# Kernel optimization log

Hardware: AMD Instinct MI355X
Metric: run time of the kernel (lower is better)

Reference implementation:

```python
import jax, jax.numpy as jnp
import numpy as np

NUM_HEADS = 16
HEAD_DIM = 128
EMBED_DIM = 2048
BASE = 10000.0


def rope(x, offset=0):
    # x: [b, h, n, d]  rotary positional embedding (lrpe_type=1)
    d = x.shape[-1]
    n = x.shape[-2]
    inv_freq = 1.0 / (BASE ** (jnp.arange(0, d, 2, dtype=jnp.float32) / d))  # [d/2]
    pos = jnp.arange(n, dtype=jnp.float32) + offset                          # [n]
    ang = pos[:, None] * inv_freq[None, :]                                   # [n, d/2]
    cos, sin = jnp.cos(ang), jnp.sin(ang)
    x1, x2 = x[..., 0::2], x[..., 1::2]
    out1 = x1 * cos - x2 * sin
    out2 = x1 * sin + x2 * cos
    return jnp.stack([out1, out2], axis=-1).reshape(x.shape)


def setup_inputs() -> dict:
    key = jax.random.key(0)
    ks = jax.random.split(key, 5)
    b, n = 2, 2048
    std = 0.02
    x = jax.random.normal(ks[0], (b, n, EMBED_DIM), dtype=jnp.float32)
    Wq = jax.random.normal(ks[1], (NUM_HEADS * HEAD_DIM, EMBED_DIM), dtype=jnp.float32) * std
    Wkv = jax.random.normal(ks[2], (2 * HEAD_DIM, EMBED_DIM), dtype=jnp.float32) * std
    Wkvh = jax.random.normal(ks[3], (2 * NUM_HEADS, EMBED_DIM), dtype=jnp.float32) * std
    Wo = jax.random.normal(ks[4], (EMBED_DIM, NUM_HEADS * HEAD_DIM), dtype=jnp.float32) * std
    return {"x": x, "Wq": Wq, "Wkv": Wkv, "Wkvh": Wkvh, "Wo": Wo}


def reference(x, Wq, Wkv, Wkvh, Wo):
    b, n, _ = x.shape
    h, d = NUM_HEADS, HEAD_DIM
    q = x @ Wq.T                     # [b, n, h*d]
    kv = x @ Wkv.T                   # [b, n, 2d]
    kvh = x @ Wkvh.T                 # [b, n, 2h]  (mpa_activation='none')
    k, v = kv[..., :d], kv[..., d:]
    k_head, v_head = kvh[..., :h], kvh[..., h:]
    # gate_type=0: per-token outer product broadcast of the single kv to all heads
    k = jnp.einsum('bnd,bnh->bhnd', k, k_head)
    v = jnp.einsum('bnd,bnh->bhnd', v, v_head)
    q = q.reshape(b, n, h, d).transpose(0, 2, 1, 3)  # [b, h, n, d]
    q = rope(q)
    k = rope(k)
    scale = 1.0 / jnp.sqrt(jnp.float32(d))
    scores = jnp.einsum('bhqd,bhkd->bhqk', q, k) * scale
    causal = jnp.tril(jnp.ones((n, n), dtype=bool))
    scores = jnp.where(causal, scores, -jnp.inf)
    attn = jax.nn.softmax(scores, axis=-1)
    o = jnp.einsum('bhqk,bhkd->bhqd', attn, v)
    o = o.transpose(0, 2, 1, 3).reshape(b, n, h * d)
    return o @ Wo.T
```

## Files before the change

kernel.cpp:

```cpp
#include <hip/hip_runtime.h>
#include <stdint.h>

#define BB 2
#define HH 16
#define NN 2048
#define DD 128
#define EE 2048
#define NQKV 2304

typedef short s16x8 __attribute__((ext_vector_type(8)));
typedef float fx4 __attribute__((ext_vector_type(4)));

static __device__ __forceinline__ unsigned short f2bf(float f) {
  unsigned u = __builtin_bit_cast(unsigned, f);
  u += 0x7fffu + ((u >> 16) & 1u);
  return (unsigned short)(u >> 16);
}
static __device__ __forceinline__ float bf2f(unsigned short h) {
  unsigned u = ((unsigned)h) << 16;
  return __builtin_bit_cast(float, u);
}
static __device__ __forceinline__ void gload_lds16(const void* g, void* l) {
  __builtin_amdgcn_global_load_lds(
      (const __attribute__((address_space(1))) unsigned int*)g,
      (__attribute__((address_space(3))) unsigned int*)l, 16, 0, 0);
}
static __device__ __forceinline__ unsigned cvt_pk_bf16(float lo, float hi) {
  unsigned w;
  asm("v_cvt_pk_bf16_f32 %0, %1, %2" : "=v"(w) : "v"(lo), "v"(hi));
  return w;
}

__global__ __launch_bounds__(256) void f2b_kernel(const float* __restrict__ in,
                                                  unsigned short* __restrict__ out,
                                                  int n4) {
  int i = blockIdx.x * 256 + threadIdx.x;
  if (i < n4) {
    float4 v = ((const float4*)in)[i];
    uint2 o;
    o.x = ((unsigned)f2bf(v.y) << 16) | f2bf(v.x);
    o.y = ((unsigned)f2bf(v.w) << 16) | f2bf(v.z);
    ((uint2*)out)[i] = o;
  }
}

#define GBM 128
#define GBN 128
#define GBK 32

__global__ __launch_bounds__(256) void gemm_bt(const unsigned short* __restrict__ A,
                                               const unsigned short* __restrict__ B,
                                               unsigned short* __restrict__ Cb,
                                               float* __restrict__ Cf,
                                               int M, int N, int K) {
  __shared__ alignas(16) unsigned short Alds[GBM * GBK];
  __shared__ alignas(16) unsigned short Blds[GBN * GBK];
  const int tid = threadIdx.x;
  const int wave = tid >> 6, lane = tid & 63;
  const int g = lane >> 4, lr = lane & 15;
  const int mtiles = M / GBM;
  const int mt = blockIdx.x % mtiles, nt = blockIdx.x / mtiles;
  const int m0 = mt * GBM, n0 = nt * GBN;
  const int wr = wave >> 1, wc = wave & 1;

  fx4 acc[4][4];
#pragma unroll
  for (int i = 0; i < 4; ++i)
#pragma unroll
    for (int j = 0; j < 4; ++j) acc[i][j] = (fx4){0.f, 0.f, 0.f, 0.f};

  const int srow = wave * 32 + (lane >> 2);
  const int scolb = (lane & 3) * 16;
  const unsigned char* Ag = (const unsigned char*)(A + (size_t)(m0 + srow) * K) + scolb;
  const unsigned char* Bg = (const unsigned char*)(B + (size_t)(n0 + srow) * K) + scolb;
  unsigned short* Al = Alds + wave * 32 * GBK;
  unsigned short* Bl = Blds + wave * 32 * GBK;
  const size_t rowb = (size_t)K * 2;

  for (int k0 = 0; k0 < K; k0 += GBK) {
    const unsigned char* ag = Ag + (size_t)k0 * 2;
    const unsigned char* bg = Bg + (size_t)k0 * 2;
    gload_lds16(ag, Al);
    gload_lds16(ag + 16 * rowb, Al + 16 * GBK);
    gload_lds16(bg, Bl);
    gload_lds16(bg + 16 * rowb, Bl + 16 * GBK);
    __syncthreads();
    s16x8 af[4], bf[4];
#pragma unroll
    for (int i = 0; i < 4; ++i)
      af[i] = *(const s16x8*)(Alds + (wr * 64 + i * 16 + lr) * GBK + 8 * g);
#pragma unroll
    for (int i = 0; i < 4; ++i)
      bf[i] = *(const s16x8*)(Blds + (wc * 64 + i * 16 + lr) * GBK + 8 * g);
#pragma unroll
    for (int i = 0; i < 4; ++i)
#pragma unroll
      for (int j = 0; j < 4; ++j)
        acc[i][j] = __builtin_amdgcn_mfma_f32_16x16x32_bf16(af[i], bf[j], acc[i][j], 0, 0, 0);
    __syncthreads();
  }
#pragma unroll
  for (int i = 0; i < 4; ++i) {
    int row = m0 + wr * 64 + i * 16 + 4 * g;
#pragma unroll
    for (int j = 0; j < 4; ++j) {
      int col = n0 + wc * 64 + j * 16 + lr;
#pragma unroll
      for (int r = 0; r < 4; ++r) {
        float v = acc[i][j][r];
        if (Cf) Cf[(size_t)(row + r) * N + col] = v;
        else    Cb[(size_t)(row + r) * N + col] = f2bf(v);
      }
    }
  }
}

__global__ __launch_bounds__(256) void kvh_mfma(const unsigned short* __restrict__ X,
                                                const unsigned short* __restrict__ Wb,
                                                float* __restrict__ out) {
  const int tid = threadIdx.x;
  const int wave = tid >> 6, lane = tid & 63;
  const int g = lane >> 4, lr = lane & 15;
  const int rowbase = blockIdx.x * 32 + (wave & 1) * 16;
  const int colbase = (wave >> 1) * 16;

  const unsigned short* xr = X + (size_t)(rowbase + lr) * EE + 8 * g;
  const unsigned short* wr = Wb + (size_t)(colbase + lr) * EE + 8 * g;

  fx4 acc = (fx4){0.f, 0.f, 0.f, 0.f};
#pragma unroll 8
  for (int k0 = 0; k0 < EE; k0 += 32) {
    s16x8 a = *(const s16x8*)(xr + k0);
    s16x8 b = *(const s16x8*)(wr + k0);
    acc = __builtin_amdgcn_mfma_f32_16x16x32_bf16(a, b, acc, 0, 0, 0);
  }
  const int j = colbase + lr;
  const int head = j & 15, sel = j >> 4;
#pragma unroll
  for (int r = 0; r < 4; ++r) {
    int m = rowbase + 4 * g + r;
    int b = m >> 11, n = m & (NN - 1);
    out[(((size_t)(b * HH + head)) * NN + n) * 2 + sel] = acc[r];
  }
}

__global__ __launch_bounds__(256) void rope_q(const unsigned short* __restrict__ qp,
                                              unsigned short* __restrict__ qo) {
  int idx = blockIdx.x * 256 + threadIdx.x;
  int i = idx & 63;
  int n = (idx >> 6) & (NN - 1);
  int bh = idx >> 17;
  int b = bh >> 4, h = bh & 15;
  unsigned v = *(const unsigned*)(qp + ((size_t)(b * NN + n) * NQKV + h * DD + 2 * i));
  float x1 = bf2f((unsigned short)(v & 0xffff));
  float x2 = bf2f((unsigned short)(v >> 16));
  float inv = __expf(-0.14391156831212787f * (float)i);
  float ang = (float)n * inv;
  float sn, cs;
  __sincosf(ang, &sn, &cs);
  float o1 = x1 * cs - x2 * sn, o2 = x1 * sn + x2 * cs;
  unsigned ov = ((unsigned)f2bf(o2) << 16) | f2bf(o1);
  *(unsigned*)(qo + ((size_t)bh * NN + n) * DD + 2 * i) = ov;
}

__global__ __launch_bounds__(256) void rope_k(const unsigned short* __restrict__ qkv,
                                              unsigned short* __restrict__ ko) {
  int idx = blockIdx.x * 256 + threadIdx.x;
  int i = idx & 63;
  int bn = idx >> 6;
  int n = bn & (NN - 1);
  unsigned v = *(const unsigned*)(qkv + (size_t)bn * NQKV + 2048 + 2 * i);
  float x1 = bf2f((unsigned short)(v & 0xffff));
  float x2 = bf2f((unsigned short)(v >> 16));
  float inv = __expf(-0.14391156831212787f * (float)i);
  float ang = (float)n * inv;
  float sn, cs;
  __sincosf(ang, &sn, &cs);
  float o1 = x1 * cs - x2 * sn, o2 = x1 * sn + x2 * cs;
  unsigned ov = ((unsigned)f2bf(o2) << 16) | f2bf(o1);
  *(unsigned*)(ko + (size_t)bn * DD + 2 * i) = ov;
}

__global__ __launch_bounds__(256) void vtrans(const unsigned short* __restrict__ qkv,
                                              unsigned short* __restrict__ vT) {
  __shared__ unsigned short t[64][40];
  int bx = blockIdx.x;
  int b = bx >> 7;
  int d0 = ((bx >> 5) & 3) * 32;
  int n0 = (bx & 31) * 64;
  int tid = threadIdx.x;
  {
    int i = tid >> 2;
    int c = (tid & 3) * 8;
    s16x8 v = *(const s16x8*)(qkv + ((size_t)(b * NN + n0 + i)) * NQKV + 2048 + 128 + d0 + c);
#pragma unroll
    for (int u = 0; u < 8; ++u) t[i][c + u] = (unsigned short)v[u];
  }
  __syncthreads();
  {
    int j = tid >> 3;
    int cc = (tid & 7) * 8;
    s16x8 o;
#pragma unroll
    for (int u = 0; u < 8; ++u) o[u] = (short)t[cc + u][j];
    *(s16x8*)(vT + ((size_t)(b * DD + d0 + j)) * NN + n0 + cc) = o;
  }
}

#define QB 128
#define KB 64

__global__ __launch_bounds__(512, 2) void attn(const unsigned short* __restrict__ Q,
                                               const unsigned short* __restrict__ Kr,
                                               const unsigned short* __restrict__ VT,
                                               const float* __restrict__ KVHP,
                                               unsigned short* __restrict__ O) {
  __shared__ alignas(16) unsigned char Klds[2 * 64 * 256];
  __shared__ alignas(16) unsigned char Vlds[2 * 128 * 128];
  __shared__ alignas(16) unsigned char Plds[16 * 16 * 128];
  __shared__ float2 mlbuf[4][2][16];

  const int qp = blockIdx.x;
  const int h = blockIdx.y;
  const int b = blockIdx.z;
  const int tid = threadIdx.x;
  const int wave = tid >> 6, lane = tid & 63;
  const int parity = wave >> 2, wq = wave & 3;
  const int g = lane >> 4, lr = lane & 15;
  const size_t bh = (size_t)(b * HH + h);

  const float scale2 = 0.08838834764831845f * 1.4426950408889634f;
  const unsigned short* Kb = Kr + (size_t)b * NN * DD;
  const unsigned short* VTb = VT + (size_t)b * DD * NN;
  const float2* KVp = (const float2*)KVHP + (size_t)(b * HH + h) * NN;

  unsigned char* Kl = Klds + parity * (64 * 256);
  unsigned char* Vl = Vlds + parity * (128 * 128);
  float* Obuf = (float*)Plds;

  auto STAGE = [&](int key0s) {
#pragma unroll
    for (int j = 0; j < 4; ++j) {
      int rl = wq * 16 + j * 4 + (lane >> 4);
      int ch = (lane & 15) ^ (rl & 7);
      const unsigned char* gp = (const unsigned char*)(Kb + (size_t)(key0s + rl) * DD) + ch * 16;
      gload_lds16(gp, (void*)(Kl + (wq * 16 + j * 4) * 256));
    }
#pragma unroll
    for (int j = 0; j < 4; ++j) {
      int row = wq * 32 + j * 8 + (lane >> 3);
      int c = lane & 7;
      const unsigned short* gp = VTb + (size_t)row * NN + key0s + ((c ^ (row & 7)) * 8);
      gload_lds16(gp, (void*)(Vl + (wq * 32 + j * 8) * 128));
    }
  };

  auto PHASE = [&](int qt) {
    const int qbase_w = qt * QB + wq * 32;

    s16x8 qf[2][4];
#pragma unroll
    for (int qq = 0; qq < 2; ++qq) {
      const unsigned short* qptr = Q + (bh * NN + qbase_w + qq * 16 + lr) * DD + 8 * g;
#pragma unroll
      for (int dc = 0; dc < 4; ++dc) qf[qq][dc] = *(const s16x8*)(qptr + dc * 32);
    }

    float m_run[2] = {-1e30f, -1e30f}, l_run[2] = {0.f, 0.f};
    fx4 oacc[2][8];
#pragma unroll
    for (int qq = 0; qq < 2; ++qq)
#pragma unroll
      for (int d = 0; d < 8; ++d) oacc[qq][d] = (fx4){0.f, 0.f, 0.f, 0.f};

    const int cnt = qt + 1;
    for (int i = 0; i < cnt; ++i) {
      const int key0 = (2 * i + parity) * KB;
      __syncthreads();
      fx4 khv[4], vhv[4];
#pragma unroll
      for (int kb = 0; kb < 4; ++kb) {
        const float4* kp = (const float4*)(KVp + key0 + kb * 16 + 4 * g);
        float4 f0 = kp[0];
        float4 f1 = kp[1];
        khv[kb] = (fx4){f0.x * scale2, f0.z * scale2, f1.x * scale2, f1.z * scale2};
        vhv[kb] = (fx4){f0.y, f0.w, f1.y, f1.w};
      }
      STAGE(key0);
      __syncthreads();

      if (key0 <= qbase_w + 31) {
        fx4 sacc[2][4];
#pragma unroll
        for (int qq = 0; qq < 2; ++qq)
#pragma unroll
          for (int kb = 0; kb < 4; ++kb) sacc[qq][kb] = (fx4){0.f, 0.f, 0.f, 0.f};
        __builtin_amdgcn_s_setprio(1);
#pragma unroll
        for (int kb = 0; kb < 4; ++kb) {
#pragma unroll
          for (int dc = 0; dc < 4; ++dc) {
            int key = kb * 16 + lr;
            int chunk = (dc * 4 + g) ^ (key & 7);
            s16x8 kf = *(const s16x8*)(Kl + key * 256 + chunk * 16);
            sacc[0][kb] = __builtin_amdgcn_mfma_f32_16x16x32_bf16(kf, qf[0][dc], sacc[0][kb], 0, 0, 0);
            sacc[1][kb] = __builtin_amdgcn_mfma_f32_16x16x32_bf16(kf, qf[1][dc], sacc[1][kb], 0, 0, 0);
          }
        }
        __builtin_amdgcn_s_setprio(0);

#pragma unroll
        for (int qq = 0; qq < 2; ++qq) {
          const int qg = qbase_w + qq * 16 + lr;
          float smax = -1e30f;
          if (key0 + 63 > qbase_w + qq * 16) {
#pragma unroll
            for (int kb = 0; kb < 4; ++kb) {
#pragma unroll
              for (int r = 0; r < 4; ++r) {
                int keyg = key0 + kb * 16 + 4 * g + r;
                float s = sacc[qq][kb][r] * khv[kb][r];
                if (keyg > qg) s = -1e30f;
                sacc[qq][kb][r] = s;
                smax = fmaxf(smax, s);
              }
            }
          } else {
#pragma unroll
            for (int kb = 0; kb < 4; ++kb) {
#pragma unroll
              for (int r = 0; r < 4; ++r) {
                float s = sacc[qq][kb][r] * khv[kb][r];
                sacc[qq][kb][r] = s;
                smax = fmaxf(smax, s);
              }
            }
          }
          smax = fmaxf(smax, __shfl_xor(smax, 16));
          smax = fmaxf(smax, __shfl_xor(smax, 32));
          if (!__all(smax - m_run[qq] <= 8.0f)) {
            float mnew = fmaxf(m_run[qq], smax);
            float corr = exp2f(m_run[qq] - mnew);
            m_run[qq] = mnew;
            l_run[qq] *= corr;
            float cr[4];
#pragma unroll
            for (int r = 0; r < 4; ++r) cr[r] = __shfl(corr, 4 * g + r);
#pragma unroll
            for (int d = 0; d < 8; ++d)
#pragma unroll
              for (int r = 0; r < 4; ++r) oacc[qq][d][r] *= cr[r];
          }
          float rsum = 0.f;
#pragma unroll
          for (int kb = 0; kb < 4; ++kb) {
            float p0 = exp2f(sacc[qq][kb][0] - m_run[qq]);
            float p1 = exp2f(sacc[qq][kb][1] - m_run[qq]);
            float p2 = exp2f(sacc[qq][kb][2] - m_run[qq]);
            float p3 = exp2f(sacc[qq][kb][3] - m_run[qq]);
            rsum += (p0 + p1) + (p2 + p3);
            uint2 w;
            w.x = cvt_pk_bf16(p0 * vhv[kb][0], p1 * vhv[kb][1]);
            w.y = cvt_pk_bf16(p2 * vhv[kb][2], p3 * vhv[kb][3]);
            int chunk = (kb * 2 + (g >> 1)) ^ (lr & 7);
            *(uint2*)(Plds + (wave * 2 + qq) * 2048 + lr * 128 + chunk * 16 + (g & 1) * 8) = w;
          }
          rsum += __shfl_xor(rsum, 16);
          rsum += __shfl_xor(rsum, 32);
          l_run[qq] += rsum;
        }

        s16x8 pa[2][2];
#pragma unroll
        for (int qq = 0; qq < 2; ++qq)
#pragma unroll
          for (int kk = 0; kk < 2; ++kk) {
            int chunk = (kk * 4 + g) ^ (lr & 7);
            pa[qq][kk] = *(const s16x8*)(Plds + (wave * 2 + qq) * 2048 + lr * 128 + chunk * 16);
          }
        __builtin_amdgcn_s_setprio(1);
#pragma unroll
        for (int dc = 0; dc < 8; ++dc) {
#pragma unroll
          for (int kk = 0; kk < 2; ++kk) {
            int d = dc * 16 + lr;
            int chunk = (kk * 4 + g) ^ (d & 7);
            s16x8 vf = *(const s16x8*)(Vl + d * 128 + chunk * 16);
            oacc[0][dc] = __builtin_amdgcn_mfma_f32_16x16x32_bf16(pa[0][kk], vf, oacc[0][dc], 0, 0, 0);
            oacc[1][dc] = __builtin_amdgcn_mfma_f32_16x16x32_bf16(pa[1][kk], vf, oacc[1][dc], 0, 0, 0);
          }
        }
        __builtin_amdgcn_s_setprio(0);
      }
    }

    __syncthreads();
    if (parity == 1 && g == 0) {
#pragma unroll
      for (int qq = 0; qq < 2; ++qq)
        mlbuf[wq][qq][lr] = make_float2(m_run[qq], l_run[qq]);
    }
    __syncthreads();
    float lC[2], af0[2][4], af1[2][4];
    if (parity == 0) {
#pragma unroll
      for (int qq = 0; qq < 2; ++qq) {
        float2 ml1 = mlbuf[wq][qq][lr];
        float M = fmaxf(m_run[qq], ml1.x);
        float a0 = exp2f(m_run[qq] - M);
        float a1 = exp2f(ml1.x - M);
        lC[qq] = l_run[qq] * a0 + ml1.y * a1;
#pragma unroll
        for (int r = 0; r < 4; ++r) {
          af0[qq][r] = __shfl(a0, 4 * g + r);
          af1[qq][r] = __shfl(a1, 4 * g + r);
        }
      }
    }
#pragma unroll
    for (int dh = 0; dh < 2; ++dh) {
      if (parity == 1) {
#pragma unroll
        for (int qq = 0; qq < 2; ++qq)
#pragma unroll
          for (int dc2 = 0; dc2 < 4; ++dc2)
#pragma unroll
            for (int r = 0; r < 4; ++r)
              Obuf[wq * 2048 + (qq * 16 + 4 * g + r) * 64 + dc2 * 16 + lr] =
                  oacc[qq][dh * 4 + dc2][r];
      }
      __syncthreads();
      if (parity == 0) {
#pragma unroll
        for (int qq = 0; qq < 2; ++qq)
#pragma unroll
          for (int dc2 = 0; dc2 < 4; ++dc2)
#pragma unroll
            for (int r = 0; r < 4; ++r) {
              float o1 = Obuf[wq * 2048 + (qq * 16 + 4 * g + r) * 64 + dc2 * 16 + lr];
              oacc[qq][dh * 4 + dc2][r] =
                  oacc[qq][dh * 4 + dc2][r] * af0[qq][r] + o1 * af1[qq][r];
            }
      }
      __syncthreads();
    }
    if (parity == 0) {
#pragma unroll
      for (int qq = 0; qq < 2; ++qq) {
        float inv = 1.0f / lC[qq];
#pragma unroll
        for (int r = 0; r < 4; ++r) {
          float invr = __shfl(inv, 4 * g + r);
          int qout = qbase_w + qq * 16 + 4 * g + r;
          unsigned short* orow = O + (((size_t)b * NN + qout) * HH + h) * DD;
#pragma unroll
          for (int dc = 0; dc < 8; ++dc) orow[dc * 16 + lr] = f2bf(oacc[qq][dc][r] * invr);
        }
      }
    }
  };

  PHASE(qp);
  PHASE(15 - qp);
}

extern "C" void kernel_launch(void* const* d_in, const int* in_sizes, int n_in,
                              void* d_out, int out_size, void* d_ws, size_t ws_size,
                              hipStream_t stream) {
  const float* x = (const float*)d_in[0];
  const float* Wq = (const float*)d_in[1];
  const float* Wkv = (const float*)d_in[2];
  const float* Wkvh = (const float*)d_in[3];
  const float* Wo = (const float*)d_in[4];
  float* out = (float*)d_out;
  char* ws = (char*)d_ws;

  unsigned short* xb    = (unsigned short*)(ws + 0);
  unsigned short* obuf  = xb;
  unsigned short* wqkv  = (unsigned short*)(ws + 16777216);
  unsigned short* vtb   = wqkv;
  unsigned short* wob   = (unsigned short*)(ws + 26214400);
  unsigned short* qkv   = (unsigned short*)(ws + 34603008);
  unsigned short* wkvhb = (unsigned short*)(ws + 53477376);
  float*          kvhb  = (float*)(ws + 53608448);
  unsigned short* qrope = (unsigned short*)(ws + 54132736);
  unsigned short* krope = (unsigned short*)(ws + 70909952);

  f2b_kernel<<<8192, 256, 0, stream>>>(x, xb, 2097152);
  f2b_kernel<<<4096, 256, 0, stream>>>(Wq, wqkv, 1048576);
  f2b_kernel<<<512, 256, 0, stream>>>(Wkv, wqkv + 4194304, 131072);
  f2b_kernel<<<4096, 256, 0, stream>>>(Wo, wob, 1048576);
  f2b_kernel<<<64, 256, 0, stream>>>(Wkvh, wkvhb, 16384);

  gemm_bt<<<576, 256, 0, stream>>>(xb, wqkv, qkv, (float*)nullptr, 4096, NQKV, 2048);
  kvh_mfma<<<128, 256, 0, stream>>>(xb, wkvhb, kvhb);

  rope_q<<<16384, 256, 0, stream>>>(qkv, qrope);
  rope_k<<<1024, 256, 0, stream>>>(qkv, krope);
  vtrans<<<256, 256, 0, stream>>>(qkv, vtb);

  dim3 ag(8, HH, BB);
  attn<<<ag, 512, 0, stream>>>(qrope, krope, vtb, kvhb, obuf);

  gemm_bt<<<512, 256, 0, stream>>>(obuf, wob, (unsigned short*)nullptr, out, 4096, 2048, 2048);
}
```

Baseline: 255.3 us.

## Fuse Q RoPE into QKV GEMM epilogue and widen GEMM K-tile with swizzled LDS

The QKV projection GEMM now applies rotary embedding to the Q columns in its epilogue, using a lane shuffle to pair even and odd dims. It writes Q straight into the head-major layout, so the separate rope_q pass and the bf16 Q round-trip through memory go away. K/V go to a compact 256-wide buffer. Both GEMMs now use a 64-wide K tile with an XOR-swizzled LDS layout, which halves the barrier count per K and avoids bank conflicts, at the cost of more LDS per block. The fused epilogue does strided scattered bf16 stores and per-element sincos, which may be less efficient than the old coalesced writes.

```diff
diff --git a/kernel.cpp b/kernel.cpp
--- a/kernel.cpp
+++ b/kernel.cpp
@@ -6,7 +6,6 @@
 #define NN 2048
 #define DD 128
 #define EE 2048
-#define NQKV 2304
 
 typedef short s16x8 __attribute__((ext_vector_type(8)));
 typedef float fx4 __attribute__((ext_vector_type(4)));
@@ -44,61 +43,67 @@
   }
 }
 
-#define GBM 128
-#define GBN 128
-#define GBK 32
-
-__global__ __launch_bounds__(256) void gemm_bt(const unsigned short* __restrict__ A,
-                                               const unsigned short* __restrict__ B,
-                                               unsigned short* __restrict__ Cb,
-                                               float* __restrict__ Cf,
-                                               int M, int N, int K) {
-  __shared__ alignas(16) unsigned short Alds[GBM * GBK];
-  __shared__ alignas(16) unsigned short Blds[GBN * GBK];
-  const int tid = threadIdx.x;
-  const int wave = tid >> 6, lane = tid & 63;
-  const int g = lane >> 4, lr = lane & 15;
-  const int mtiles = M / GBM;
-  const int mt = blockIdx.x % mtiles, nt = blockIdx.x / mtiles;
-  const int m0 = mt * GBM, n0 = nt * GBN;
-  const int wr = wave >> 1, wc = wave & 1;
-
-  fx4 acc[4][4];
-#pragma unroll
-  for (int i = 0; i < 4; ++i)
-#pragma unroll
-    for (int j = 0; j < 4; ++j) acc[i][j] = (fx4){0.f, 0.f, 0.f, 0.f};
-
-  const int srow = wave * 32 + (lane >> 2);
-  const int scolb = (lane & 3) * 16;
-  const unsigned char* Ag = (const unsigned char*)(A + (size_t)(m0 + srow) * K) + scolb;
-  const unsigned char* Bg = (const unsigned char*)(B + (size_t)(n0 + srow) * K) + scolb;
-  unsigned short* Al = Alds + wave * 32 * GBK;
-  unsigned short* Bl = Blds + wave * 32 * GBK;
+#define GBK 64
+
+#define GEMM_STAGE(LDSB, SRCBASE, rowb)                                        \
+  _Pragma("unroll") for (int t = 0; t < 4; ++t) {                              \
+    int r = wave * 32 + t * 8 + (lane >> 3);                                   \
+    int ch = (lane & 7) ^ (r & 7);                                             \
+    const unsigned char* src = (SRCBASE) + (size_t)r * (rowb) + ch * 16;       \
+    gload_lds16(src, (void*)((LDSB) + (wave * 32 + t * 8) * 128));             \
+  }
+
+#define GEMM_LOOP_BODY                                                         \
+  for (int k0 = 0; k0 < K; k0 += GBK) {                                        \
+    const unsigned char* ag = Ag + (size_t)k0 * 2;                             \
+    const unsigned char* bg = Bg + (size_t)k0 * 2;                             \
+    __syncthreads();                                                           \
+    GEMM_STAGE(Alds, ag, rowb)                                                 \
+    GEMM_STAGE(Blds, bg, rowb)                                                 \
+    __syncthreads();                                                           \
+    _Pragma("unroll") for (int kk = 0; kk < 2; ++kk) {                         \
+      s16x8 af[4], bf[4];                                                      \
+      _Pragma("unroll") for (int i = 0; i < 4; ++i) {                          \
+        int row = wr * 64 + i * 16 + lr;                                       \
+        int chunk = (kk * 4 + g) ^ (row & 7);                                  \
+        af[i] = *(const s16x8*)(Alds + row * 128 + chunk * 16);                \
+      }                                                                        \
+      _Pragma("unroll") for (int j = 0; j < 4; ++j) {                          \
+        int row = wc * 64 + j * 16 + lr;                                       \
+        int chunk = (kk * 4 + g) ^ (row & 7);                                  \
+        bf[j] = *(const s16x8*)(Blds + row * 128 + chunk * 16);                \
+      }                                                                        \
+      _Pragma("unroll") for (int i = 0; i < 4; ++i)                            \
+        _Pragma("unroll") for (int j = 0; j < 4; ++j)                          \
+          acc[i][j] = __builtin_amdgcn_mfma_f32_16x16x32_bf16(af[i], bf[j],    \
+                                                              acc[i][j], 0, 0, 0); \
+    }                                                                          \
+  }
+
+#define GEMM_PROLOG                                                            \
+  __shared__ alignas(16) unsigned char Alds[128 * 128];                        \
+  __shared__ alignas(16) unsigned char Blds[128 * 128];                        \
+  const int tid = threadIdx.x;                                                 \
+  const int wave = tid >> 6, lane = tid & 63;                                  \
+  const int g = lane >> 4, lr = lane & 15;                                     \
+  const int mtiles = M / 128;                                                  \
+  const int mt = blockIdx.x % mtiles, nt = blockIdx.x / mtiles;                \
+  const int m0 = mt * 128, n0 = nt * 128;                                      \
+  const int wr = wave >> 1, wc = wave & 1;                                     \
+  fx4 acc[4][4];                                                               \
+  _Pragma("unroll") for (int i = 0; i < 4; ++i)                                \
+    _Pragma("unroll") for (int j = 0; j < 4; ++j)                              \
+      acc[i][j] = (fx4){0.f, 0.f, 0.f, 0.f};                                   \
+  const unsigned char* Ag = (const unsigned char*)(A + (size_t)m0 * K);        \
+  const unsigned char* Bg = (const unsigned char*)(B + (size_t)n0 * K);        \
   const size_t rowb = (size_t)K * 2;
 
-  for (int k0 = 0; k0 < K; k0 += GBK) {
-    const unsigned char* ag = Ag + (size_t)k0 * 2;
-    const unsigned char* bg = Bg + (size_t)k0 * 2;
-    gload_lds16(ag, Al);
-    gload_lds16(ag + 16 * rowb, Al + 16 * GBK);
-    gload_lds16(bg, Bl);
-    gload_lds16(bg + 16 * rowb, Bl + 16 * GBK);
-    __syncthreads();
-    s16x8 af[4], bf[4];
-#pragma unroll
-    for (int i = 0; i < 4; ++i)
-      af[i] = *(const s16x8*)(Alds + (wr * 64 + i * 16 + lr) * GBK + 8 * g);
-#pragma unroll
-    for (int i = 0; i < 4; ++i)
-      bf[i] = *(const s16x8*)(Blds + (wc * 64 + i * 16 + lr) * GBK + 8 * g);
-#pragma unroll
-    for (int i = 0; i < 4; ++i)
-#pragma unroll
-      for (int j = 0; j < 4; ++j)
-        acc[i][j] = __builtin_amdgcn_mfma_f32_16x16x32_bf16(af[i], bf[j], acc[i][j], 0, 0, 0);
-    __syncthreads();
-  }
+__global__ __launch_bounds__(256) void gemm_out(const unsigned short* __restrict__ A,
+                                                const unsigned short* __restrict__ B,
+                                                float* __restrict__ Cf,
+                                                int M, int N, int K) {
+  GEMM_PROLOG
+  GEMM_LOOP_BODY
 #pragma unroll
   for (int i = 0; i < 4; ++i) {
     int row = m0 + wr * 64 + i * 16 + 4 * g;
@@ -106,10 +111,50 @@
     for (int j = 0; j < 4; ++j) {
       int col = n0 + wc * 64 + j * 16 + lr;
 #pragma unroll
-      for (int r = 0; r < 4; ++r) {
-        float v = acc[i][j][r];
-        if (Cf) Cf[(size_t)(row + r) * N + col] = v;
-        else    Cb[(size_t)(row + r) * N + col] = f2bf(v);
+      for (int r = 0; r < 4; ++r)
+        Cf[(size_t)(row + r) * N + col] = acc[i][j][r];
+    }
+  }
+}
+
+__global__ __launch_bounds__(256) void gemm_qkv(const unsigned short* __restrict__ A,
+                                                const unsigned short* __restrict__ B,
+                                                unsigned short* __restrict__ qrope,
+                                                unsigned short* __restrict__ kvb,
+                                                int M, int N, int K) {
+  GEMM_PROLOG
+  GEMM_LOOP_BODY
+#pragma unroll
+  for (int j = 0; j < 4; ++j) {
+    int col = n0 + wc * 64 + j * 16 + lr;
+    if (col < 2048) {
+      int hh = col >> 7, d = col & 127;
+      float invf = __expf(-0.14391156831212787f * (float)(d >> 1));
+      int par = d & 1;
+#pragma unroll
+      for (int i = 0; i < 4; ++i) {
+#pragma unroll
+        for (int r = 0; r < 4; ++r) {
+          int row = m0 + wr * 64 + i * 16 + 4 * g + r;
+          int n = row & (NN - 1), bq = row >> 11;
+          float self = acc[i][j][r];
+          float other = __shfl_xor(self, 1);
+          float sn, cs;
+          __sincosf((float)n * invf, &sn, &cs);
+          float a = self * cs, bt = other * sn;
+          float o = par ? (a + bt) : (a - bt);
+          qrope[((size_t)(bq * HH + hh) * NN + n) * DD + d] = f2bf(o);
+        }
+      }
+    } else {
+      int c2 = col - 2048;
+#pragma unroll
+      for (int i = 0; i < 4; ++i) {
+#pragma unroll
+        for (int r = 0; r < 4; ++r) {
+          int row = m0 + wr * 64 + i * 16 + 4 * g + r;
+          kvb[(size_t)row * 256 + c2] = f2bf(acc[i][j][r]);
+        }
       }
     }
   }
@@ -144,32 +189,13 @@
   }
 }
 
-__global__ __launch_bounds__(256) void rope_q(const unsigned short* __restrict__ qp,
-                                              unsigned short* __restrict__ qo) {
-  int idx = blockIdx.x * 256 + threadIdx.x;
-  int i = idx & 63;
-  int n = (idx >> 6) & (NN - 1);
-  int bh = idx >> 17;
-  int b = bh >> 4, h = bh & 15;
-  unsigned v = *(const unsigned*)(qp + ((size_t)(b * NN + n) * NQKV + h * DD + 2 * i));
-  float x1 = bf2f((unsigned short)(v & 0xffff));
-  float x2 = bf2f((unsigned short)(v >> 16));
-  float inv = __expf(-0.14391156831212787f * (float)i);
-  float ang = (float)n * inv;
-  float sn, cs;
-  __sincosf(ang, &sn, &cs);
-  float o1 = x1 * cs - x2 * sn, o2 = x1 * sn + x2 * cs;
-  unsigned ov = ((unsigned)f2bf(o2) << 16) | f2bf(o1);
-  *(unsigned*)(qo + ((size_t)bh * NN + n) * DD + 2 * i) = ov;
-}
-
-__global__ __launch_bounds__(256) void rope_k(const unsigned short* __restrict__ qkv,
+__global__ __launch_bounds__(256) void rope_k(const unsigned short* __restrict__ kv,
                                               unsigned short* __restrict__ ko) {
   int idx = blockIdx.x * 256 + threadIdx.x;
   int i = idx & 63;
   int bn = idx >> 6;
   int n = bn & (NN - 1);
-  unsigned v = *(const unsigned*)(qkv + (size_t)bn * NQKV + 2048 + 2 * i);
+  unsigned v = *(const unsigned*)(kv + (size_t)bn * 256 + 2 * i);
   float x1 = bf2f((unsigned short)(v & 0xffff));
   float x2 = bf2f((unsigned short)(v >> 16));
   float inv = __expf(-0.14391156831212787f * (float)i);
@@ -181,7 +207,7 @@
   *(unsigned*)(ko + (size_t)bn * DD + 2 * i) = ov;
 }
 
-__global__ __launch_bounds__(256) void vtrans(const unsigned short* __restrict__ qkv,
+__global__ __launch_bounds__(256) void vtrans(const unsigned short* __restrict__ kv,
                                               unsigned short* __restrict__ vT) {
   __shared__ unsigned short t[64][40];
   int bx = blockIdx.x;
@@ -192,7 +218,7 @@
   {
     int i = tid >> 2;
     int c = (tid & 3) * 8;
-    s16x8 v = *(const s16x8*)(qkv + ((size_t)(b * NN + n0 + i)) * NQKV + 2048 + 128 + d0 + c);
+    s16x8 v = *(const s16x8*)(kv + ((size_t)(b * NN + n0 + i)) * 256 + 128 + d0 + c);
 #pragma unroll
     for (int u = 0; u < 8; ++u) t[i][c + u] = (unsigned short)v[u];
   }
@@ -480,7 +506,7 @@
   unsigned short* wqkv  = (unsigned short*)(ws + 16777216);
   unsigned short* vtb   = wqkv;
   unsigned short* wob   = (unsigned short*)(ws + 26214400);
-  unsigned short* qkv   = (unsigned short*)(ws + 34603008);
+  unsigned short* kvb   = (unsigned short*)(ws + 34603008);
   unsigned short* wkvhb = (unsigned short*)(ws + 53477376);
   float*          kvhb  = (float*)(ws + 53608448);
   unsigned short* qrope = (unsigned short*)(ws + 54132736);
@@ -492,15 +518,14 @@
   f2b_kernel<<<4096, 256, 0, stream>>>(Wo, wob, 1048576);
   f2b_kernel<<<64, 256, 0, stream>>>(Wkvh, wkvhb, 16384);
 
-  gemm_bt<<<576, 256, 0, stream>>>(xb, wqkv, qkv, (float*)nullptr, 4096, NQKV, 2048);
+  gemm_qkv<<<576, 256, 0, stream>>>(xb, wqkv, qrope, kvb, 4096, 2304, 2048);
   kvh_mfma<<<128, 256, 0, stream>>>(xb, wkvhb, kvhb);
 
-  rope_q<<<16384, 256, 0, stream>>>(qkv, qrope);
-  rope_k<<<1024, 256, 0, stream>>>(qkv, krope);
-  vtrans<<<256, 256, 0, stream>>>(qkv, vtb);
+  rope_k<<<1024, 256, 0, stream>>>(kvb, krope);
+  vtrans<<<256, 256, 0, stream>>>(kvb, vtb);
 
   dim3 ag(8, HH, BB);
   attn<<<ag, 512, 0, stream>>>(qrope, krope, vtb, kvhb, obuf);
 
-  gemm_bt<<<512, 256, 0, stream>>>(obuf, wob, (unsigned short*)nullptr, out, 4096, 2048, 2048);
-}
+  gemm_out<<<512, 256, 0, stream>>>(obuf, wob, out, 4096, 2048, 2048);
+}
```

After: 221.0 us. 1.16x faster.
